# Performance work log

Hardware: AMD Instinct MI355X
Metric: run time of the kernel (lower is better)

## Reference

```python
import jax, jax.numpy as jnp
import numpy as np

# norse LIFParameters defaults with method='super', alpha=100
TAU_SYN_INV = 200.0
TAU_MEM_INV = 100.0
V_LEAK = 0.0
V_TH = 1.0
V_RESET = 0.0
ALPHA = 100.0
DT = 0.001
SEQ_LENGTH = 100

@jax.custom_vjp
def super_spike(x):
    return (x > 0).astype(x.dtype)

def _ss_fwd(x):
    return super_spike(x), x

def _ss_bwd(x, g):
    # SuperSpike surrogate: dz/dx = 1 / (alpha*|x| + 1)^2
    return (g / (ALPHA * jnp.abs(x) + 1.0) ** 2,)

super_spike.defvjp(_ss_fwd, _ss_bwd)

def lif_step(inp, v, i):
    v_dec = v + DT * TAU_MEM_INV * ((V_LEAK - v) + i)
    i_dec = i * (1.0 - DT * TAU_SYN_INV)
    z = super_spike(v_dec - V_TH)
    v_new = (1.0 - z) * v_dec + z * V_RESET
    i_new = i_dec + inp
    return z, v_new, i_new

def setup_inputs() -> dict:
    key = jax.random.key(0)
    ks = jax.random.split(key, 5)
    B, F, H, C = 16384, 256, 256, 10
    x = jax.random.normal(ks[0], (B, F), dtype=jnp.float32)
    W_hidden = jax.random.normal(ks[1], (H, F), dtype=jnp.float32) / np.sqrt(F)
    b_hidden = jax.random.normal(ks[2], (H,), dtype=jnp.float32) * 0.01
    W_readout = jax.random.normal(ks[3], (C, H), dtype=jnp.float32) / np.sqrt(H)
    b_readout = jax.random.normal(ks[4], (C,), dtype=jnp.float32) * 0.01
    return {"x": x, "W_hidden": W_hidden, "b_hidden": b_hidden,
            "W_readout": W_readout, "b_readout": b_readout}

def reference(x, W_hidden, b_hidden, W_readout, b_readout):
    B, F = x.shape
    H = W_hidden.shape[0]
    z0 = jnp.zeros((B, F), x.dtype)
    z1 = jnp.zeros((B, H), x.dtype)

    def step(carry, _):
        v1, i1, v2, i2, acc = carry
        # input LIF cell (same input current x at every timestep)
        z, v1, i1 = lif_step(x, v1, i1)
        h = jnp.einsum('bf,hf->bh', z, W_hidden) + b_hidden
        # output LIF cell
        z2, v2, i2 = lif_step(h, v2, i2)
        return (v1, i1, v2, i2, acc + z2), None

    carry0 = (z0, z0, z1, z1, z1)
    (v1, i1, v2, i2, acc), _ = jax.lax.scan(step, carry0, None, length=SEQ_LENGTH)
    mean_spikes = acc / SEQ_LENGTH  # == outputs.mean(0)
    return jnp.einsum('bh,ch->bc', mean_spikes, W_readout) + b_readout
```

## Files before the change

### kernel.cpp

```cpp
#include <hip/hip_runtime.h>
#include <hip/hip_fp16.h>
#include <stdint.h>


#define BB 16384
#define FF 256
#define HH 256
#define CC 10
#define TT 100

typedef __attribute__((ext_vector_type(4))) int int4v;

__global__ __launch_bounds__(256) void spike_gen(
    const float* __restrict__ x, unsigned long long* __restrict__ Z) {
  const int lane = threadIdx.x & 63;
  const int wv   = threadIdx.x >> 6;
  const int b0   = blockIdx.x * 16 + wv * 4;
  const float K_VM = (float)(0.001 * 100.0);
  const float K_ID = (float)(1.0 - 0.001 * 200.0);

  float v[16], cur[16], xv[16];
#pragma unroll
  for (int jb = 0; jb < 4; ++jb)
#pragma unroll
    for (int js = 0; js < 4; ++js) {
      const int idx = jb * 4 + js;
      xv[idx] = x[(size_t)(b0 + jb) * FF + js * 64 + lane];
      v[idx] = 0.0f; cur[idx] = 0.0f;
    }

  unsigned long long mymask = 0;
  unsigned long long* zp = Z + (size_t)b0 * 4;

  for (int t = 0; t < TT; ++t) {
#pragma unroll
    for (int idx = 0; idx < 16; ++idx) {
      float vd   = __fadd_rn(v[idx], __fmul_rn(K_VM, __fadd_rn(-v[idx], cur[idx])));
      float idec = __fmul_rn(cur[idx], K_ID);
      bool z = (vd > 1.0f);
      unsigned long long m = __ballot(z);
      if (lane == idx) mymask = m;
      v[idx]   = z ? 0.0f : vd;
      cur[idx] = __fadd_rn(idec, xv[idx]);
    }
    if (lane < 16) zp[(size_t)t * (BB * 4) + lane] = mymask;
  }
}

__global__ __launch_bounds__(256, 2) void snn_main(
    const uint32_t* __restrict__ Z, const float* __restrict__ Wh,
    const float* __restrict__ bh, const float* __restrict__ Wr,
    const float* __restrict__ br, float* __restrict__ out) {
  __shared__ __align__(16) char WS[32768];

  const int tid = threadIdx.x;
  const int bx  = blockIdx.x;
  const int hc  = bx & 3;
  const int bc  = bx >> 2;
  const int h0  = hc * 64;
  const int b0  = bc * 64;

  {
    const int r = tid & 63;
    const int w = tid >> 6;
    const int nt = r >> 4, n = r & 15;
    const float* wrow = Wh + (size_t)(h0 + r) * FF + w * 64;
    int4v* ws4 = (int4v*)WS;
#pragma unroll
    for (int q = 0; q < 4; ++q) {
      uint32_t pa[4], pb[4];
#pragma unroll
      for (int c4 = 0; c4 < 4; ++c4) {
        float4 w4 = *(const float4*)(wrow + q * 16 + c4 * 4);
        float wf[4] = {w4.x, w4.y, w4.z, w4.w};
        uint32_t ua = 0, ub = 0;
#pragma unroll
        for (int e = 0; e < 4; ++e) {
          float af = rintf(wf[e] * 256.0f);
          af = fminf(fmaxf(af, -127.0f), 127.0f);
          float bf = rintf(__builtin_fmaf(af, -64.0f, wf[e] * 16384.0f));
          int ai = (int)af, bi = (int)bf;
          ua |= ((uint32_t)ai & 255u) << (8 * e);
          ub |= ((uint32_t)bi & 255u) << (8 * e);
        }
        pa[c4] = ua; pb[c4] = ub;
      }
      ws4[((nt * 2 + 0) * 4 + w) * 64 + q * 16 + n] = *(int4v*)pa;
      ws4[((nt * 2 + 1) * 4 + w) * 64 + q * 16 + n] = *(int4v*)pb;
    }
  }
  __syncthreads();

  const int lane = tid & 63;
  const int wv   = tid >> 6;
  const int col  = lane & 15;
  const int quad = lane >> 4;
  const bool qhi = (quad & 2) != 0;
  const uint32_t shl16 = (quad & 1) * 16;

  const int brow = b0 + wv * 16 + col;

  const float K_VM = (float)(0.001 * 100.0);
  const float K_ID = (float)(1.0 - 0.001 * 200.0);

  float v2[4][4], ii[4][4];
  uint32_t sc[4][4];
#pragma unroll
  for (int nt = 0; nt < 4; ++nt)
#pragma unroll
    for (int r = 0; r < 4; ++r) { v2[nt][r] = 0.f; ii[nt][r] = 0.f; sc[nt][r] = 0u; }

  float bias[4];
#pragma unroll
  for (int nt = 0; nt < 4; ++nt) bias[nt] = bh[h0 + nt * 16 + col];

  uint32_t hwS0[4], hwS1[4], hwS2[4], hwS3[4];
  const uint32_t* zrow = Z + (size_t)brow * 8;

  auto load_hw = [&](int tgi) {
#pragma unroll
    for (int j = 0; j < 4; ++j) {
      const uint32_t* p = zrow + ((size_t)tgi * 4 + j) * (size_t)(BB * 8);
      uint4 a = *(const uint4*)p;
      uint4 b4 = *(const uint4*)(p + 4);
      hwS0[j] = (qhi ? a.y : a.x) >> shl16;
      hwS1[j] = (qhi ? a.w : a.z) >> shl16;
      hwS2[j] = (qhi ? b4.y : b4.x) >> shl16;
      hwS3[j] = (qhi ? b4.w : b4.z) >> shl16;
    }
  };
  load_hw(0);

  const char* wsl = WS + lane * 16;

#pragma unroll 1
  for (int tg = 0; tg < TT / 4; ++tg) {
    int4v acc[4][4];
#pragma unroll
    for (int j = 0; j < 4; ++j)
#pragma unroll
      for (int nt = 0; nt < 4; ++nt)
        acc[j][nt] = (int4v){0, 0, 0, 0};

#pragma unroll 1
    for (int s = 0; s < 4; ++s) {
      const int4v* bp = (const int4v*)(wsl + s * 1024);
      int4v Ba[4], Bb[4];
#pragma unroll
      for (int nt = 0; nt < 4; ++nt) {
        Ba[nt] = bp[(nt * 2 + 0) * 256];
        Bb[nt] = bp[(nt * 2 + 1) * 256];
      }
#pragma unroll
      for (int j = 0; j < 4; ++j) {
        uint32_t t0 = (s & 1) ? hwS1[j] : hwS0[j];
        uint32_t t1 = (s & 1) ? hwS3[j] : hwS2[j];
        uint32_t h16 = (s & 2) ? t1 : t0;
        int4v za, zb_;
#pragma unroll
        for (int p = 0; p < 4; ++p) {
          uint32_t nib = (h16 >> (4 * p)) & 15u;
          uint32_t zbyte = (nib * 0x204081u) & 0x01010101u;
          zb_[p] = (int)zbyte;
          za[p]  = (int)(zbyte << 6);
        }
#pragma unroll
        for (int nt = 0; nt < 4; ++nt) {
          acc[j][nt] = __builtin_amdgcn_mfma_i32_16x16x64_i8(
              za, Ba[nt], acc[j][nt], 0, 0, 0);
          acc[j][nt] = __builtin_amdgcn_mfma_i32_16x16x64_i8(
              zb_, Bb[nt], acc[j][nt], 0, 0, 0);
        }
      }
    }

    if (tg < TT / 4 - 1) load_hw(tg + 1);

#pragma unroll
    for (int j = 0; j < 4; ++j) {
#pragma unroll
      for (int nt = 0; nt < 4; ++nt) {
#pragma unroll
        for (int r = 0; r < 4; ++r) {
          float hq = __fmul_rn((float)acc[j][nt][r], 6.103515625e-05f);
          float h  = __fadd_rn(hq, bias[nt]);
          float vv = v2[nt][r], ci = ii[nt][r];
          float vd   = __fadd_rn(vv, __fmul_rn(K_VM, __fadd_rn(-vv, ci)));
          float idec = __fmul_rn(ci, K_ID);
          bool z = (vd > 1.0f);
          v2[nt][r] = z ? 0.0f : vd;
          ii[nt][r] = __fadd_rn(idec, h);
          sc[nt][r] += z ? 1u : 0u;
        }
      }
    }
  }

  float mean[4][4];
#pragma unroll
  for (int nt = 0; nt < 4; ++nt)
#pragma unroll
    for (int r = 0; r < 4; ++r) mean[nt][r] = __fdiv_rn((float)sc[nt][r], 100.0f);

#pragma unroll 1
  for (int c = 0; c < CC; ++c) {
    float wc[4];
#pragma unroll
    for (int nt = 0; nt < 4; ++nt) wc[nt] = Wr[c * HH + h0 + nt * 16 + col];
#pragma unroll
    for (int r = 0; r < 4; ++r) {
      float s = 0.f;
#pragma unroll
      for (int nt = 0; nt < 4; ++nt) s = fmaf(mean[nt][r], wc[nt], s);
      s += __shfl_xor(s, 1);
      s += __shfl_xor(s, 2);
      s += __shfl_xor(s, 4);
      s += __shfl_xor(s, 8);
      if (col == 0) {
        int b = b0 + wv * 16 + quad * 4 + r;
        float add = s + ((hc == 0) ? br[c] : 0.0f);
        atomicAdd(&out[b * CC + c], add);
      }
    }
  }
}

extern "C" void kernel_launch(void* const* d_in, const int* in_sizes, int n_in,
                              void* d_out, int out_size, void* d_ws, size_t ws_size,
                              hipStream_t stream) {
  const float* x  = (const float*)d_in[0];
  const float* Wh = (const float*)d_in[1];
  const float* bh = (const float*)d_in[2];
  const float* Wr = (const float*)d_in[3];
  const float* br = (const float*)d_in[4];
  float* out = (float*)d_out;

  unsigned long long* Z = (unsigned long long*)d_ws;

  hipMemsetAsync(d_out, 0, (size_t)out_size * sizeof(float), stream);
  spike_gen<<<BB / 16, 256, 0, stream>>>(x, Z);
  snn_main<<<(BB / 64) * 4, 256, 0, stream>>>((const uint32_t*)Z, Wh, bh, Wr, br, out);
}
```

Baseline: 433.9 us.

## Halve per-thread state in both kernels to raise occupancy

The spike generator now handles 2 batch rows per wave instead of 4 and launches twice as many blocks. Its ballot results are selected with a log-depth select tree instead of a per-lane conditional assignment. The main kernel processes timesteps in groups of 2 instead of 4, packs its spike counters into bytes, and uses a fused multiply-add for dequantisation, all to cut registers and allow 4 blocks per CU. The weight-quantisation prologue is remapped across all threads, and the low-byte term is now clamped. The trade-off is more loop iterations with less MFMA work each, and slightly different float rounding from the FMA.

```diff
diff --git a/kernel.cpp b/kernel.cpp
--- a/kernel.cpp
+++ b/kernel.cpp
@@ -15,13 +15,13 @@
     const float* __restrict__ x, unsigned long long* __restrict__ Z) {
   const int lane = threadIdx.x & 63;
   const int wv   = threadIdx.x >> 6;
-  const int b0   = blockIdx.x * 16 + wv * 4;
+  const int b0   = blockIdx.x * 8 + wv * 2;
   const float K_VM = (float)(0.001 * 100.0);
   const float K_ID = (float)(1.0 - 0.001 * 200.0);
 
-  float v[16], cur[16], xv[16];
-#pragma unroll
-  for (int jb = 0; jb < 4; ++jb)
+  float v[8], cur[8], xv[8];
+#pragma unroll
+  for (int jb = 0; jb < 2; ++jb)
 #pragma unroll
     for (int js = 0; js < 4; ++js) {
       const int idx = jb * 4 + js;
@@ -29,25 +29,32 @@
       v[idx] = 0.0f; cur[idx] = 0.0f;
     }
 
-  unsigned long long mymask = 0;
+  const bool s0 = (lane & 1) != 0, s1 = (lane & 2) != 0, s2 = (lane & 4) != 0;
   unsigned long long* zp = Z + (size_t)b0 * 4;
 
   for (int t = 0; t < TT; ++t) {
-#pragma unroll
-    for (int idx = 0; idx < 16; ++idx) {
+    unsigned long long bal[8];
+#pragma unroll
+    for (int idx = 0; idx < 8; ++idx) {
       float vd   = __fadd_rn(v[idx], __fmul_rn(K_VM, __fadd_rn(-v[idx], cur[idx])));
       float idec = __fmul_rn(cur[idx], K_ID);
       bool z = (vd > 1.0f);
-      unsigned long long m = __ballot(z);
-      if (lane == idx) mymask = m;
+      bal[idx] = __ballot(z);
       v[idx]   = z ? 0.0f : vd;
       cur[idx] = __fadd_rn(idec, xv[idx]);
     }
-    if (lane < 16) zp[(size_t)t * (BB * 4) + lane] = mymask;
+    unsigned long long m0 = s0 ? bal[1] : bal[0];
+    unsigned long long m1 = s0 ? bal[3] : bal[2];
+    unsigned long long m2 = s0 ? bal[5] : bal[4];
+    unsigned long long m3 = s0 ? bal[7] : bal[6];
+    unsigned long long n0 = s1 ? m1 : m0;
+    unsigned long long n1 = s1 ? m3 : m2;
+    unsigned long long m  = s2 ? n1 : n0;
+    if (lane < 8) zp[(size_t)t * (BB * 4) + lane] = m;
   }
 }
 
-__global__ __launch_bounds__(256, 2) void snn_main(
+__global__ __launch_bounds__(256, 4) void snn_main(
     const uint32_t* __restrict__ Z, const float* __restrict__ Wh,
     const float* __restrict__ bh, const float* __restrict__ Wr,
     const float* __restrict__ br, float* __restrict__ out) {
@@ -61,17 +68,19 @@
   const int b0  = bc * 64;
 
   {
-    const int r = tid & 63;
-    const int w = tid >> 6;
-    const int nt = r >> 4, n = r & 15;
-    const float* wrow = Wh + (size_t)(h0 + r) * FF + w * 64;
     int4v* ws4 = (int4v*)WS;
 #pragma unroll
-    for (int q = 0; q < 4; ++q) {
+    for (int half = 0; half < 4; ++half) {
+      const int u  = tid + half * 256;
+      const int rr = u >> 4;
+      const int q  = u & 15;
+      const int s  = q >> 2, kq = q & 3;
+      const int nt = rr >> 4, n = rr & 15;
+      const float* wp = Wh + (size_t)(h0 + rr) * FF + s * 64 + kq * 16;
       uint32_t pa[4], pb[4];
 #pragma unroll
       for (int c4 = 0; c4 < 4; ++c4) {
-        float4 w4 = *(const float4*)(wrow + q * 16 + c4 * 4);
+        float4 w4 = *(const float4*)(wp + c4 * 4);
         float wf[4] = {w4.x, w4.y, w4.z, w4.w};
         uint32_t ua = 0, ub = 0;
 #pragma unroll
@@ -79,48 +88,50 @@
           float af = rintf(wf[e] * 256.0f);
           af = fminf(fmaxf(af, -127.0f), 127.0f);
           float bf = rintf(__builtin_fmaf(af, -64.0f, wf[e] * 16384.0f));
-          int ai = (int)af, bi = (int)bf;
-          ua |= ((uint32_t)ai & 255u) << (8 * e);
-          ub |= ((uint32_t)bi & 255u) << (8 * e);
+          bf = fminf(fmaxf(bf, -127.0f), 127.0f);
+          ua |= ((uint32_t)((int)af) & 255u) << (8 * e);
+          ub |= ((uint32_t)((int)bf) & 255u) << (8 * e);
         }
         pa[c4] = ua; pb[c4] = ub;
       }
-      ws4[((nt * 2 + 0) * 4 + w) * 64 + q * 16 + n] = *(int4v*)pa;
-      ws4[((nt * 2 + 1) * 4 + w) * 64 + q * 16 + n] = *(int4v*)pb;
+      ws4[((nt * 2 + 0) * 4 + s) * 64 + kq * 16 + n] = *(int4v*)pa;
+      ws4[((nt * 2 + 1) * 4 + s) * 64 + kq * 16 + n] = *(int4v*)pb;
     }
   }
   __syncthreads();
 
   const int lane = tid & 63;
-  const int wv   = tid >> 6;
+  const int bsub = tid >> 6;
   const int col  = lane & 15;
   const int quad = lane >> 4;
   const bool qhi = (quad & 2) != 0;
   const uint32_t shl16 = (quad & 1) * 16;
 
-  const int brow = b0 + wv * 16 + col;
+  const int brow = b0 + bsub * 16 + col;
 
   const float K_VM = (float)(0.001 * 100.0);
   const float K_ID = (float)(1.0 - 0.001 * 200.0);
 
   float v2[4][4], ii[4][4];
-  uint32_t sc[4][4];
-#pragma unroll
-  for (int nt = 0; nt < 4; ++nt)
-#pragma unroll
-    for (int r = 0; r < 4; ++r) { v2[nt][r] = 0.f; ii[nt][r] = 0.f; sc[nt][r] = 0u; }
+  uint32_t sc[4];
+#pragma unroll
+  for (int nt = 0; nt < 4; ++nt) {
+    sc[nt] = 0u;
+#pragma unroll
+    for (int r = 0; r < 4; ++r) { v2[nt][r] = 0.f; ii[nt][r] = 0.f; }
+  }
 
   float bias[4];
 #pragma unroll
   for (int nt = 0; nt < 4; ++nt) bias[nt] = bh[h0 + nt * 16 + col];
 
-  uint32_t hwS0[4], hwS1[4], hwS2[4], hwS3[4];
+  uint32_t hwS0[2], hwS1[2], hwS2[2], hwS3[2];
   const uint32_t* zrow = Z + (size_t)brow * 8;
 
   auto load_hw = [&](int tgi) {
 #pragma unroll
-    for (int j = 0; j < 4; ++j) {
-      const uint32_t* p = zrow + ((size_t)tgi * 4 + j) * (size_t)(BB * 8);
+    for (int j = 0; j < 2; ++j) {
+      const uint32_t* p = zrow + ((size_t)tgi * 2 + j) * (size_t)(BB * 8);
       uint4 a = *(const uint4*)p;
       uint4 b4 = *(const uint4*)(p + 4);
       hwS0[j] = (qhi ? a.y : a.x) >> shl16;
@@ -134,10 +145,10 @@
   const char* wsl = WS + lane * 16;
 
 #pragma unroll 1
-  for (int tg = 0; tg < TT / 4; ++tg) {
-    int4v acc[4][4];
-#pragma unroll
-    for (int j = 0; j < 4; ++j)
+  for (int tg = 0; tg < TT / 2; ++tg) {
+    int4v acc[2][4];
+#pragma unroll
+    for (int j = 0; j < 2; ++j)
 #pragma unroll
       for (int nt = 0; nt < 4; ++nt)
         acc[j][nt] = (int4v){0, 0, 0, 0};
@@ -152,7 +163,7 @@
         Bb[nt] = bp[(nt * 2 + 1) * 256];
       }
 #pragma unroll
-      for (int j = 0; j < 4; ++j) {
+      for (int j = 0; j < 2; ++j) {
         uint32_t t0 = (s & 1) ? hwS1[j] : hwS0[j];
         uint32_t t1 = (s & 1) ? hwS3[j] : hwS2[j];
         uint32_t h16 = (s & 2) ? t1 : t0;
@@ -160,7 +171,7 @@
 #pragma unroll
         for (int p = 0; p < 4; ++p) {
           uint32_t nib = (h16 >> (4 * p)) & 15u;
-          uint32_t zbyte = (nib * 0x204081u) & 0x01010101u;
+          uint32_t zbyte = __umul24(nib, 0x204081u) & 0x01010101u;
           zb_[p] = (int)zbyte;
           za[p]  = (int)(zbyte << 6);
         }
@@ -174,23 +185,23 @@
       }
     }
 
-    if (tg < TT / 4 - 1) load_hw(tg + 1);
-
-#pragma unroll
-    for (int j = 0; j < 4; ++j) {
+    if (tg < TT / 2 - 1) load_hw(tg + 1);
+
+#pragma unroll
+    for (int j = 0; j < 2; ++j) {
 #pragma unroll
       for (int nt = 0; nt < 4; ++nt) {
 #pragma unroll
         for (int r = 0; r < 4; ++r) {
-          float hq = __fmul_rn((float)acc[j][nt][r], 6.103515625e-05f);
-          float h  = __fadd_rn(hq, bias[nt]);
+          float h  = __builtin_fmaf((float)acc[j][nt][r], 6.103515625e-05f,
+                                    bias[nt]);
           float vv = v2[nt][r], ci = ii[nt][r];
           float vd   = __fadd_rn(vv, __fmul_rn(K_VM, __fadd_rn(-vv, ci)));
           float idec = __fmul_rn(ci, K_ID);
           bool z = (vd > 1.0f);
           v2[nt][r] = z ? 0.0f : vd;
           ii[nt][r] = __fadd_rn(idec, h);
-          sc[nt][r] += z ? 1u : 0u;
+          sc[nt] += (z ? 1u : 0u) << (8 * r);
         }
       }
     }
@@ -200,7 +211,8 @@
 #pragma unroll
   for (int nt = 0; nt < 4; ++nt)
 #pragma unroll
-    for (int r = 0; r < 4; ++r) mean[nt][r] = __fdiv_rn((float)sc[nt][r], 100.0f);
+    for (int r = 0; r < 4; ++r)
+      mean[nt][r] = __fdiv_rn((float)((sc[nt] >> (8 * r)) & 255u), 100.0f);
 
 #pragma unroll 1
   for (int c = 0; c < CC; ++c) {
@@ -217,7 +229,7 @@
       s += __shfl_xor(s, 4);
       s += __shfl_xor(s, 8);
       if (col == 0) {
-        int b = b0 + wv * 16 + quad * 4 + r;
+        int b = b0 + bsub * 16 + quad * 4 + r;
         float add = s + ((hc == 0) ? br[c] : 0.0f);
         atomicAdd(&out[b * CC + c], add);
       }
@@ -238,6 +250,6 @@
   unsigned long long* Z = (unsigned long long*)d_ws;
 
   hipMemsetAsync(d_out, 0, (size_t)out_size * sizeof(float), stream);
-  spike_gen<<<BB / 16, 256, 0, stream>>>(x, Z);
-  snn_main<<<(BB / 64) * 4, 256, 0, stream>>>((const uint32_t*)Z, Wh, bh, Wr, br, out);
+  spike_gen<<<BB / 8, 256, 0, stream>>>(x, Z);
+  snn_main<<<1024, 256, 0, stream>>>((const uint32_t*)Z, Wh, bh, Wr, br, out);
 }
```

Measured after the change: 389.8 us. 1.11x faster.
